# Performance work log

Hardware: AMD Instinct MI355X
Metric: run time of the kernel (lower is better)

The kernel has to match this reference:

```python
import jax, jax.numpy as jnp
import numpy as np

MAX_LEN = 960
EMB = 200
SQRT_DK = np.sqrt(MAX_LEN).astype(np.float32)  # note: sqrt(max_len), as in source


def setup_inputs() -> dict:
    key = jax.random.key(0)
    k1, k2, k3, k4 = jax.random.split(key, 4)
    B, S, F = 16, 2048, 800
    x = jax.random.normal(k1, (B, S, F), dtype=jnp.float32)
    # torch Linear(960,200) weight init scale ~ 1/sqrt(960); random normal scaled
    scale = 1.0 / np.sqrt(MAX_LEN)
    Wq = jax.random.normal(k2, (MAX_LEN, EMB), dtype=jnp.float32) * scale
    Wk = jax.random.normal(k3, (MAX_LEN, EMB), dtype=jnp.float32) * scale
    Wv = jax.random.normal(k4, (MAX_LEN, EMB), dtype=jnp.float32) * scale
    return {"x": x, "Wq": Wq, "Wk": Wk, "Wv": Wv}


def reference(x, Wq, Wk, Wv):
    # pad feature dim up to MAX_LEN with zeros
    pad = MAX_LEN - x.shape[2]
    x = jnp.pad(x, ((0, 0), (0, 0), (0, pad)))
    gelu = lambda t: jax.nn.gelu(t, approximate=False)  # torch nn.GELU default = exact
    q = gelu(jnp.einsum('bsf,fe->bse', x, Wq))  # [B,S,E]
    k = gelu(jnp.einsum('bsf,fe->bse', x, Wk))
    v = gelu(jnp.einsum('bsf,fe->bse', x, Wv))
    score = jnp.einsum('bqe,bke->bqk', q, k) / SQRT_DK  # [B,S,S]
    attn = jax.nn.softmax(score, axis=-1)
    return jnp.einsum('bqk,bke->bqe', attn, v)  # [B,S,E]
```

## Files before the change

kernel.cpp:

```cpp
#include <hip/hip_runtime.h>
#include <hip/hip_bf16.h>

#define B_  16
#define S_  2048
#define F_  800
#define E_  200
#define EP  224
#define KP  832
#define KSP 256
#define M_  (B_ * S_)

typedef __attribute__((ext_vector_type(8))) short short8;
typedef __attribute__((ext_vector_type(4))) float f32x4;

#define QSCL (0.03227486121839514f * 1.4426950408889634f)

__device__ __forceinline__ unsigned short f2bf(float f) {
    __hip_bfloat16 h = __float2bfloat16(f);
    return *reinterpret_cast<unsigned short*>(&h);
}

__device__ __forceinline__ float exp2_fast(float x) {
    float r;
    asm("v_exp_f32 %0, %1" : "=v"(r) : "v"(x));
    return r;
}

__device__ __forceinline__ float rcp_fast(float x) {
    float r;
    asm("v_rcp_f32 %0, %1" : "=v"(r) : "v"(x));
    return r;
}

__device__ __forceinline__ float gelu_fast(float x) {
    const float i = x + 0.044715f * x * x * x;
    const float z = 2.302265314f * i;
    return x * rcp_fast(1.0f + exp2_fast(-z));
}

__device__ __forceinline__ void gload_lds16(const void* g, void* l) {
    __builtin_amdgcn_global_load_lds(
        (const __attribute__((address_space(1))) unsigned int*)g,
        (__attribute__((address_space(3))) unsigned int*)l, 16, 0, 0);
}

__global__ __launch_bounds__(256)
void prep_x(const float* __restrict__ x, unsigned short* __restrict__ xb) {
    const int id = blockIdx.x * 256 + threadIdx.x;
    const int r  = id / (KP / 8);
    const int c8 = id % (KP / 8);
    ushort4 lo = {0, 0, 0, 0}, hi = {0, 0, 0, 0};
    if (c8 < F_ / 8) {
        const float4 a = *reinterpret_cast<const float4*>(x + (size_t)r * F_ + c8 * 8);
        const float4 b = *reinterpret_cast<const float4*>(x + (size_t)r * F_ + c8 * 8 + 4);
        lo.x = f2bf(a.x); lo.y = f2bf(a.y); lo.z = f2bf(a.z); lo.w = f2bf(a.w);
        hi.x = f2bf(b.x); hi.y = f2bf(b.y); hi.z = f2bf(b.z); hi.w = f2bf(b.w);
    }
    unsigned short* dst = xb + (size_t)r * KP + c8 * 8;
    *reinterpret_cast<ushort4*>(dst) = lo;
    *reinterpret_cast<ushort4*>(dst + 4) = hi;
}

__global__ __launch_bounds__(256)
void prep_w(const float* __restrict__ Wq, const float* __restrict__ Wk,
            const float* __restrict__ Wv, unsigned short* __restrict__ wt) {
    const int id = blockIdx.x * 256 + threadIdx.x;
    const int sel = id / (EP * KP);
    const int rem = id % (EP * KP);
    const int e = rem / KP;
    const int k = rem % KP;
    const float* W = (sel == 0) ? Wq : ((sel == 1) ? Wk : Wv);
    float v = (e < E_ && k < F_) ? W[(size_t)k * E_ + e] : 0.0f;
    wt[id] = f2bf(v);
}

#define STAGE(XB, WB, KK) do {                                                   \
    const int k0s = (KK) * 32;                                                   \
    _Pragma("unroll")                                                            \
    for (int i = 0; i < 2; ++i) {                                                \
        const int j = w * 2 + i;                                                 \
        const int row = 16 * j + rS;                                             \
        gload_lds16(xb + (size_t)(m0 + row) * KP + k0s + ((pS ^ (row & 3)) * 8), \
                    &XB[j * 512]);                                               \
    }                                                                            \
    _Pragma("unroll")                                                            \
    for (int i = 0; i < 4; ++i) {                                                \
        const int j = i * 4 + w;                                                 \
        if (j < 14) {                                                            \
            const int row = 16 * j + rS;                                         \
            gload_lds16(wsel + (size_t)row * KP + k0s + ((pS ^ (row & 3)) * 8),  \
                        &WB[j * 512]);                                           \
        }                                                                        \
    }                                                                            \
} while (0)

#define COMPUTE(XB, WB) do {                                                     \
    short8 afr[4];                                                               \
    _Pragma("unroll")                                                            \
    for (int rf = 0; rf < 4; ++rf) {                                             \
        const int row = wr * 64 + rf * 16 + ln15;                                \
        afr[rf] = *reinterpret_cast<const short8*>(                              \
            &XB[row * 32 + ((g ^ (row & 3)) * 8)]);                              \
    }                                                                            \
    _Pragma("unroll")                                                            \
    for (int cf = 0; cf < 7; ++cf) {                                             \
        const int row = wc * 112 + cf * 16 + ln15;                               \
        short8 bfr = *reinterpret_cast<const short8*>(                           \
            &WB[row * 32 + ((g ^ (row & 3)) * 8)]);                              \
        _Pragma("unroll")                                                        \
        for (int rf = 0; rf < 4; ++rf)                                           \
            acc[rf][cf] = __builtin_amdgcn_mfma_f32_16x16x32_bf16(               \
                afr[rf], bfr, acc[rf][cf], 0, 0, 0);                             \
    }                                                                            \
} while (0)

__global__ __launch_bounds__(256, 2)
void gemm_qkv(const unsigned short* __restrict__ xb,
              const unsigned short* __restrict__ wt,
              unsigned short* __restrict__ qbuf,
              unsigned short* __restrict__ kbuf,
              unsigned short* __restrict__ vtbuf) {
    const int sel = blockIdx.y;
    const int m0 = blockIdx.x * 128;
    const int t = threadIdx.x;
    const int lane = t & 63;
    const int w = t >> 6;
    const int wr = w >> 1;
    const int wc = w & 1;
    const int ln15 = lane & 15;
    const int g = lane >> 4;

    __shared__ __align__(16) unsigned short X0s[128 * 32];
    __shared__ __align__(16) unsigned short W0s[224 * 32];
    __shared__ __align__(16) unsigned short X1s[128 * 32];
    __shared__ __align__(16) unsigned short W1s[224 * 32];

    const unsigned short* wsel = wt + (size_t)sel * EP * KP;

    f32x4 acc[4][7];
#pragma unroll
    for (int i = 0; i < 4; ++i)
#pragma unroll
        for (int j = 0; j < 7; ++j) acc[i][j] = (f32x4)0.0f;

    const int rS = lane >> 2;
    const int pS = lane & 3;

    STAGE(X0s, W0s, 0);
    __syncthreads();
#pragma unroll
    for (int p = 0; p < 12; ++p) {
        STAGE(X1s, W1s, 2 * p + 1);
        COMPUTE(X0s, W0s);
        __syncthreads();
        STAGE(X0s, W0s, 2 * p + 2);
        COMPUTE(X1s, W1s);
        __syncthreads();
    }
    STAGE(X1s, W1s, 25);
    COMPUTE(X0s, W0s);
    __syncthreads();
    COMPUTE(X1s, W1s);

#pragma unroll
    for (int rf = 0; rf < 4; ++rf) {
        const int row = m0 + wr * 64 + rf * 16 + g * 4;
#pragma unroll
        for (int cf = 0; cf < 7; ++cf) {
            const int col = wc * 112 + cf * 16 + ln15;
            if (sel == 0) {
#pragma unroll
                for (int tt = 0; tt < 4; ++tt)
                    qbuf[(size_t)(row + tt) * EP + col] =
                        f2bf(gelu_fast(acc[rf][cf][tt]) * QSCL);
            } else if (sel == 1) {
#pragma unroll
                for (int tt = 0; tt < 4; ++tt)
                    kbuf[(size_t)(row + tt) * KSP + col] = f2bf(gelu_fast(acc[rf][cf][tt]));
            } else {
                const int bb = row >> 11, s = row & 2047;
                ushort4 pk;
                if (col == 200) {
                    pk.x = 0x3F80; pk.y = 0x3F80; pk.z = 0x3F80; pk.w = 0x3F80;
                } else {
                    pk.x = f2bf(gelu_fast(acc[rf][cf][0]));
                    pk.y = f2bf(gelu_fast(acc[rf][cf][1]));
                    pk.z = f2bf(gelu_fast(acc[rf][cf][2]));
                    pk.w = f2bf(gelu_fast(acc[rf][cf][3]));
                }
                *reinterpret_cast<ushort4*>(
                    &vtbuf[((size_t)(bb * EP + col)) * S_ + s]) = pk;
            }
        }
    }
}

#define BQ  128
#define BKV 64

#define ASTAGE(KB, VB, KT) do {                                                  \
    const int kv0s = (KT) * BKV;                                                 \
    {                            \
        const int r_in = lane >> 5;                                              \
        const int p = lane & 31;                                                 \
        _Pragma("unroll")                                                        \
        for (int i = 0; i < 4; ++i) {                                            \
            const int j = w * 4 + i;                                             \
            const int row = 2 * j + r_in;                                        \
            gload_lds16(kb_b + (size_t)(kv0s + row) * KSP + ((p ^ (row & 7)) * 8),\
                        &KB[j * 512]);                                           \
        }                                                                        \
    }                                                                            \
    {                                        \
        const int r_in = lane >> 3;                                              \
        const int p = lane & 7;                                                  \
        _Pragma("unroll")                                                        \
        for (int i = 0; i < 4; ++i) {                                            \
            const int j = i * 8 + w;                                             \
            if (j < 28) {                                                        \
                const int row = 8 * j + r_in;                                    \
                gload_lds16(vt_b + (size_t)row * S_ + kv0s + ((p ^ (row & 7)) * 8),\
                            &VB[j * 512]);                                       \
            }                                                                    \
        }                                                                        \
    }                                                                            \
} while (0)

#define ACOMPUTE(KB, VB) do {                                                    \
    f32x4 sacc[4];                                                               \
    _Pragma("unroll")                                                            \
    for (int n = 0; n < 4; ++n) {                                                \
        f32x4 a = (f32x4)0.0f;                                                   \
        const int krow = n * 16 + ln15;                                          \
        const unsigned short* kr = &KB[krow * KSP];                              \
        const int rx = krow & 7;                                                 \
        _Pragma("unroll")                                                        \
        for (int s = 0; s < 7; ++s) {                                            \
            short8 bf = *reinterpret_cast<const short8*>(                        \
                kr + (((s * 4 + g) ^ rx) * 8));                                  \
            a = __builtin_amdgcn_mfma_f32_16x16x32_bf16(qf[s], bf, a, 0, 0, 0);  \
        }                                                                        \
        sacc[n] = a;                                                             \
    }                                                                            \
    _Pragma("unroll")                                                            \
    for (int n = 0; n < 4; ++n)                                                  \
        _Pragma("unroll")                                                        \
        for (int tt = 0; tt < 4; ++tt)                                           \
            Plds[w][g * 4 + tt][n * 16 + ln15] = f2bf(exp2_fast(sacc[n][tt]));   \
    short8 pf0 = *reinterpret_cast<const short8*>(&Plds[w][ln15][g * 8]);        \
    short8 pf1 = *reinterpret_cast<const short8*>(&Plds[w][ln15][32 + g * 8]);   \
    _Pragma("unroll")                                                            \
    for (int n = 0; n < 14; ++n) {                                               \
        const int vrow = n * 16 + ln15;                                          \
        const unsigned short* vr = &VB[vrow * 64];                               \
        const int rx = vrow & 7;                                                 \
        short8 b0 = *reinterpret_cast<const short8*>(vr + ((g ^ rx) * 8));       \
        short8 b1 = *reinterpret_cast<const short8*>(vr + (((4 + g) ^ rx) * 8)); \
        o[n] = __builtin_amdgcn_mfma_f32_16x16x32_bf16(pf0, b0, o[n], 0, 0, 0);  \
        o[n] = __builtin_amdgcn_mfma_f32_16x16x32_bf16(pf1, b1, o[n], 0, 0, 0);  \
    }                                                                            \
} while (0)

__global__ __launch_bounds__(512, 2)
void attn_kernel(const unsigned short* __restrict__ qbuf,
                 const unsigned short* __restrict__ kbuf,
                 const unsigned short* __restrict__ vtbuf,
                 float* __restrict__ out) {
    const int id = blockIdx.x;
    const int slot = id >> 3;
    const int b = 2 * (id & 7) + (slot >> 4);
    const int q0 = (slot & 15) * BQ;
    const int t = threadIdx.x;
    const int lane = t & 63;
    const int w = t >> 6;
    const int ln15 = lane & 15;
    const int g = lane >> 4;

    __shared__ __align__(16) unsigned short Ks[2][BKV * KSP];
    __shared__ __align__(16) unsigned short Vts[2][EP * 64];
    __shared__ __align__(16) unsigned short Plds[8][16][68];

    short8 qf[7];
    {
        const unsigned short* qp =
            qbuf + (size_t)(b * S_ + q0 + w * 16 + ln15) * EP + g * 8;
#pragma unroll
        for (int s = 0; s < 7; ++s)
            qf[s] = *reinterpret_cast<const short8*>(qp + s * 32);
    }

    f32x4 o[14];
#pragma unroll
    for (int i = 0; i < 14; ++i) o[i] = (f32x4)0.0f;

    const unsigned short* kb_b = kbuf + (size_t)b * S_ * KSP;
    const unsigned short* vt_b = vtbuf + (size_t)b * EP * S_;

    ASTAGE(Ks[0], Vts[0], 0);
    __syncthreads();
    for (int kt = 0; kt < S_ / BKV - 1; ++kt) {
        const int cur = kt & 1;
        ASTAGE(Ks[cur ^ 1], Vts[cur ^ 1], kt + 1);
        ACOMPUTE(Ks[cur], Vts[cur]);
        __syncthreads();
    }
    ACOMPUTE(Ks[1], Vts[1]);

    {
        float l[4];
#pragma unroll
        for (int tt = 0; tt < 4; ++tt)
            l[tt] = __shfl(o[12][tt], (lane & 48) + 8, 64);
#pragma unroll
        for (int tt = 0; tt < 4; ++tt) {
            const float inv = 1.0f / l[tt];
            const int row = q0 + w * 16 + g * 4 + tt;
            float* op = out + (size_t)(b * S_ + row) * E_;
#pragma unroll
            for (int n = 0; n < 13; ++n) {
                const int e = n * 16 + ln15;
                if (e < E_) op[e] = o[n][tt] * inv;
            }
        }
    }
}

extern "C" void kernel_launch(void* const* d_in, const int* in_sizes, int n_in,
                              void* d_out, int out_size, void* d_ws, size_t ws_size,
                              hipStream_t stream) {
    const float* x  = (const float*)d_in[0];
    const float* Wq = (const float*)d_in[1];
    const float* Wk = (const float*)d_in[2];
    const float* Wv = (const float*)d_in[3];
    float* out = (float*)d_out;

    unsigned short* xb    = (unsigned short*)d_ws;
    unsigned short* wt    = xb + (size_t)M_ * KP;
    unsigned short* qbuf  = wt + (size_t)3 * EP * KP;
    unsigned short* kbuf  = qbuf + (size_t)M_ * EP;
    unsigned short* vtbuf = kbuf + (size_t)M_ * KSP;

    prep_x<<<dim3(M_ * (KP / 8) / 256), 256, 0, stream>>>(x, xb);
    prep_w<<<dim3(3 * EP * KP / 256), 256, 0, stream>>>(Wq, Wk, Wv, wt);
    gemm_qkv<<<dim3(256, 3), 256, 0, stream>>>(xb, wt, qbuf, kbuf, vtbuf);
    attn_kernel<<<dim3(256), 512, 0, stream>>>(qbuf, kbuf, vtbuf, out);
}
```

Baseline: 170.0 us.

## Read V directly from global memory and halve attention query tile

Stops staging V tiles in LDS: each wave now loads V^T fragments for the PV MFMAs straight from global memory, while only K is double-buffered through LDS with a wider XOR swizzle. The query tile shrinks from 128 to 64 rows and blocks go from 512 to 256 threads, doubling the grid to 512 blocks. This frees LDS and cuts LDS traffic, which may let more blocks fit per CU. In exchange every wave re-reads V from L2/global with uncoalesced-ish per-lane loads, and there are more redundant K/V reads across the larger grid.

```diff
diff --git a/kernel.cpp b/kernel.cpp
--- a/kernel.cpp
+++ b/kernel.cpp
@@ -195,45 +195,31 @@
     }
 }
 
-#define BQ  128
+#define BQ  64
 #define BKV 64
 
-#define ASTAGE(KB, VB, KT) do {                                                  \
+#define ASTAGE(KB, KT) do {                                                      \
     const int kv0s = (KT) * BKV;                                                 \
-    {                            \
-        const int r_in = lane >> 5;                                              \
-        const int p = lane & 31;                                                 \
-        _Pragma("unroll")                                                        \
-        for (int i = 0; i < 4; ++i) {                                            \
-            const int j = w * 4 + i;                                             \
-            const int row = 2 * j + r_in;                                        \
-            gload_lds16(kb_b + (size_t)(kv0s + row) * KSP + ((p ^ (row & 7)) * 8),\
-                        &KB[j * 512]);                                           \
-        }                                                                        \
-    }                                                                            \
-    {                                        \
-        const int r_in = lane >> 3;                                              \
-        const int p = lane & 7;                                                  \
-        _Pragma("unroll")                                                        \
-        for (int i = 0; i < 4; ++i) {                                            \
-            const int j = i * 8 + w;                                             \
-            if (j < 28) {                                                        \
-                const int row = 8 * j + r_in;                                    \
-                gload_lds16(vt_b + (size_t)row * S_ + kv0s + ((p ^ (row & 7)) * 8),\
-                            &VB[j * 512]);                                       \
-            }                                                                    \
-        }                                                                        \
+    const int r_in = lane >> 5;                                                  \
+    const int p = lane & 31;                                                     \
+    _Pragma("unroll")                                                            \
+    for (int i = 0; i < 8; ++i) {                                                \
+        const int j = w * 8 + i;                                                 \
+        const int row = 2 * j + r_in;                                            \
+        gload_lds16(kb_b + (size_t)(kv0s + row) * KSP + ((p ^ ((row << 2) & 31)) * 8),\
+                    &KB[j * 512]);                                               \
     }                                                                            \
 } while (0)
 
-#define ACOMPUTE(KB, VB) do {                                                    \
+#define ACOMPUTE(KB, KT) do {                                                    \
+    const int kv0s = (KT) * BKV;                                                 \
     f32x4 sacc[4];                                                               \
     _Pragma("unroll")                                                            \
     for (int n = 0; n < 4; ++n) {                                                \
         f32x4 a = (f32x4)0.0f;                                                   \
         const int krow = n * 16 + ln15;                                          \
         const unsigned short* kr = &KB[krow * KSP];                              \
-        const int rx = krow & 7;                                                 \
+        const int rx = (krow << 2) & 31;                                         \
         _Pragma("unroll")                                                        \
         for (int s = 0; s < 7; ++s) {                                            \
             short8 bf = *reinterpret_cast<const short8*>(                        \
@@ -252,24 +238,23 @@
     _Pragma("unroll")                                                            \
     for (int n = 0; n < 14; ++n) {                                               \
         const int vrow = n * 16 + ln15;                                          \
-        const unsigned short* vr = &VB[vrow * 64];                               \
-        const int rx = vrow & 7;                                                 \
-        short8 b0 = *reinterpret_cast<const short8*>(vr + ((g ^ rx) * 8));       \
-        short8 b1 = *reinterpret_cast<const short8*>(vr + (((4 + g) ^ rx) * 8)); \
+        const unsigned short* vr = vt_b + (size_t)vrow * S_ + kv0s;              \
+        short8 b0 = *reinterpret_cast<const short8*>(vr + g * 8);                \
+        short8 b1 = *reinterpret_cast<const short8*>(vr + 32 + g * 8);           \
         o[n] = __builtin_amdgcn_mfma_f32_16x16x32_bf16(pf0, b0, o[n], 0, 0, 0);  \
         o[n] = __builtin_amdgcn_mfma_f32_16x16x32_bf16(pf1, b1, o[n], 0, 0, 0);  \
     }                                                                            \
 } while (0)
 
-__global__ __launch_bounds__(512, 2)
+__global__ __launch_bounds__(256, 2)
 void attn_kernel(const unsigned short* __restrict__ qbuf,
                  const unsigned short* __restrict__ kbuf,
                  const unsigned short* __restrict__ vtbuf,
                  float* __restrict__ out) {
     const int id = blockIdx.x;
     const int slot = id >> 3;
-    const int b = 2 * (id & 7) + (slot >> 4);
-    const int q0 = (slot & 15) * BQ;
+    const int b = 2 * (id & 7) + (slot >> 5);
+    const int q0 = (slot & 31) * BQ;
     const int t = threadIdx.x;
     const int lane = t & 63;
     const int w = t >> 6;
@@ -277,8 +262,7 @@
     const int g = lane >> 4;
 
     __shared__ __align__(16) unsigned short Ks[2][BKV * KSP];
-    __shared__ __align__(16) unsigned short Vts[2][EP * 64];
-    __shared__ __align__(16) unsigned short Plds[8][16][68];
+    __shared__ __align__(16) unsigned short Plds[4][16][68];
 
     short8 qf[7];
     {
@@ -296,15 +280,15 @@
     const unsigned short* kb_b = kbuf + (size_t)b * S_ * KSP;
     const unsigned short* vt_b = vtbuf + (size_t)b * EP * S_;
 
-    ASTAGE(Ks[0], Vts[0], 0);
+    ASTAGE(Ks[0], 0);
     __syncthreads();
     for (int kt = 0; kt < S_ / BKV - 1; ++kt) {
         const int cur = kt & 1;
-        ASTAGE(Ks[cur ^ 1], Vts[cur ^ 1], kt + 1);
-        ACOMPUTE(Ks[cur], Vts[cur]);
+        ASTAGE(Ks[cur ^ 1], kt + 1);
+        ACOMPUTE(Ks[cur], kt);
         __syncthreads();
     }
-    ACOMPUTE(Ks[1], Vts[1]);
+    ACOMPUTE(Ks[1], S_ / BKV - 1);
 
     {
         float l[4];
@@ -343,5 +327,5 @@
     prep_x<<<dim3(M_ * (KP / 8) / 256), 256, 0, stream>>>(x, xb);
     prep_w<<<dim3(3 * EP * KP / 256), 256, 0, stream>>>(Wq, Wk, Wv, wt);
     gemm_qkv<<<dim3(256, 3), 256, 0, stream>>>(xb, wt, qbuf, kbuf, vtbuf);
-    attn_kernel<<<dim3(256), 512, 0, stream>>>(qbuf, kbuf, vtbuf, out);
-}
+    attn_kernel<<<dim3((S_ / BQ) * B_), 256, 0, stream>>>(qbuf, kbuf, vtbuf, out);
+}
```

New measurement: 294.9 us. +73.5%, slower.
